# Kernel optimization log

Hardware: AMD Instinct MI355X
Metric: run time of the kernel (lower is better)

Reference implementation:

```python
import jax, jax.numpy as jnp
import numpy as np

R = 16
ALPHA = 16.0
SCALE = ALPHA / max(1, R)  # alpha / max(1, r)


def setup_inputs() -> dict:
    key = jax.random.key(0)
    k1, k2, k3, k4, k5 = jax.random.split(key, 5)
    B, S, D_IN, D_OUT = 4, 4096, 4096, 4096
    x = jax.random.normal(k1, (B, S, D_IN), dtype=jnp.float32)
    weight = jax.random.normal(k2, (D_OUT, D_IN), dtype=jnp.float32) * (1.0 / np.sqrt(D_IN))
    bias = jax.random.normal(k3, (D_OUT,), dtype=jnp.float32)
    lora_A = jax.random.normal(k4, (R, D_IN), dtype=jnp.float32) * (1.0 / np.sqrt(D_IN))
    lora_B = jax.random.normal(k5, (D_OUT, R), dtype=jnp.float32) * (1.0 / np.sqrt(R))
    return {"x": x, "weight": weight, "bias": bias, "lora_A": lora_A, "lora_B": lora_B}


def reference(x, weight, bias, lora_A, lora_B):
    # base = F.linear(x, weight, bias) = x @ W^T + b
    base = jnp.einsum('bsi,oi->bso', x, weight) + bias
    # lora = x @ (B @ A)^T = (x @ A^T) @ B^T  (chained low-rank, same math)
    xa = jnp.einsum('bsi,ri->bsr', x, lora_A)   # [B,S,r]
    lora = jnp.einsum('bsr,or->bso', xa, lora_B)  # [B,S,out]
    return base + SCALE * lora
```

## Files before the change

kernel.cpp:

```cpp
#include <hip/hip_runtime.h>
#include <stdint.h>

#define M_DIM 16384
#define N_DIM 4096
#define K_DIM 4096
#define LORA_SCALE 1.0f

#define BM 256
#define BN 256
#define BK 64
#define NT (K_DIM / BK)

typedef _Float16 half8 __attribute__((ext_vector_type(8)));
typedef float f32x4 __attribute__((ext_vector_type(4)));

__global__ __launch_bounds__(256) void prep_kernel(const float* __restrict__ x,
                                                   _Float16* __restrict__ xb,
                                                   const float* __restrict__ W,
                                                   const float* __restrict__ lA,
                                                   const float* __restrict__ lB,
                                                   _Float16* __restrict__ wp) {
    const int t = threadIdx.x;
    const int WBLK = (N_DIM * K_DIM) / (256 * 8);

    if (blockIdx.x < WBLK) {
        const size_t base = ((size_t)blockIdx.x * 256 + t) * 8;
        const int n = (int)(base >> 12);
        const int k = (int)(base & (K_DIM - 1));
        const int ns = __builtin_amdgcn_readfirstlane(n);
        float Brow[16];
#pragma unroll
        for (int r = 0; r < 16; ++r) Brow[r] = lB[(size_t)ns * 16 + r];

        f32x4 w0 = *(const f32x4*)(W + base);
        f32x4 w1 = *(const f32x4*)(W + base + 4);
        f32x4 d0 = {0.f, 0.f, 0.f, 0.f}, d1 = {0.f, 0.f, 0.f, 0.f};
#pragma unroll
        for (int r = 0; r < 16; ++r) {
            const float* ar = lA + (size_t)r * K_DIM + k;
            f32x4 a0 = *(const f32x4*)ar;
            f32x4 a1 = *(const f32x4*)(ar + 4);
            d0 += Brow[r] * a0;
            d1 += Brow[r] * a1;
        }
        w0 += LORA_SCALE * d0;
        w1 += LORA_SCALE * d1;
        half8 h;
        h[0] = (_Float16)w0[0]; h[1] = (_Float16)w0[1];
        h[2] = (_Float16)w0[2]; h[3] = (_Float16)w0[3];
        h[4] = (_Float16)w1[0]; h[5] = (_Float16)w1[1];
        h[6] = (_Float16)w1[2]; h[7] = (_Float16)w1[3];
        *(half8*)(wp + base) = h;
        return;
    }

    const size_t base = ((size_t)(blockIdx.x - WBLK) * 256 + t) * 8;
    f32x4 a = *(const f32x4*)(x + base);
    f32x4 b = *(const f32x4*)(x + base + 4);
    half8 h;
    h[0] = (_Float16)a[0]; h[1] = (_Float16)a[1];
    h[2] = (_Float16)a[2]; h[3] = (_Float16)a[3];
    h[4] = (_Float16)b[0]; h[5] = (_Float16)b[1];
    h[6] = (_Float16)b[2]; h[7] = (_Float16)b[3];
    *(half8*)(xb + base) = h;
}

__device__ __forceinline__ void load_lds16(const void* g, void* l) {
    __builtin_amdgcn_global_load_lds(
        (const __attribute__((address_space(1))) unsigned int*)(uintptr_t)g,
        (__attribute__((address_space(3))) unsigned int*)(uintptr_t)l,
        16, 0, 0);
}

__global__ __launch_bounds__(512, 2) void gemm256_kernel(const _Float16* __restrict__ A,
                                                         const _Float16* __restrict__ B,
                                                         const float* __restrict__ bias,
                                                         float* __restrict__ C) {
    __shared__ _Float16 As[2][2][256 * 32];
    __shared__ _Float16 Bs[2][2][256 * 32];

    const int tid  = threadIdx.x;
    const int lane = tid & 63;
    const int wave = tid >> 6;
    const int wm   = wave >> 2;
    const int wn   = wave & 3;
    const int quad = lane >> 4;
    const int r16  = lane & 15;
    const int swz  = (quad ^ ((r16 >> 1) & 3)) << 3;

    const int bid = blockIdx.x;
    const int id  = (bid & 7) * 128 + (bid >> 3);
    const int m0  = (id >> 4) * BM;
    const int n0  = (id & 15) * BN;

    const int  srow = tid >> 2;
    const int  scol = (((tid & 3) ^ ((tid >> 3) & 3)) << 3);
    const _Float16* gA = A + (size_t)(m0 + srow) * K_DIM + scol;
    const _Float16* gB = B + (size_t)(n0 + srow) * K_DIM + scol;
    const int ldst0 = tid * 8;
    const int ldst1 = (tid + 512) * 8;

    const int arow = (wm * 128 + r16) * 32 + swz;
    const int brow = (wn * 64 + r16) * 32 + swz;

    f32x4 acc[8][4] = {};
    half8 a[4], b[4];

#define ISSUE_A(DB, KH, T) do { \
        const _Float16* g_ = gA + (size_t)((T) * 64 + (KH) * 32); \
        load_lds16(g_, &As[DB][KH][ldst0]); \
        load_lds16(g_ + (size_t)128 * K_DIM, &As[DB][KH][ldst1]); \
    } while (0)
#define ISSUE_B(DB, KH, T) do { \
        const _Float16* g_ = gB + (size_t)((T) * 64 + (KH) * 32); \
        load_lds16(g_, &Bs[DB][KH][ldst0]); \
        load_lds16(g_ + (size_t)128 * K_DIM, &Bs[DB][KH][ldst1]); \
    } while (0)

#define MID() do { \
        asm volatile("" ::: "memory"); __builtin_amdgcn_sched_barrier(0); \
        __builtin_amdgcn_s_barrier(); \
        asm volatile("s_waitcnt lgkmcnt(0)" ::: "memory"); \
        __builtin_amdgcn_sched_barrier(0); \
        __builtin_amdgcn_s_setprio(1); \
    } while (0)
#define ENDP() do { \
        __builtin_amdgcn_s_setprio(0); \
        asm volatile("" ::: "memory"); __builtin_amdgcn_sched_barrier(0); \
        __builtin_amdgcn_s_barrier(); \
    } while (0)

#define MFMA16(MLO) \
        _Pragma("unroll") \
        for (int i_ = 0; i_ < 4; ++i_) \
            _Pragma("unroll") \
            for (int j_ = 0; j_ < 4; ++j_) \
                acc[(MLO) + i_][j_] = __builtin_amdgcn_mfma_f32_16x16x32_f16( \
                    a[i_], b[j_], acc[(MLO) + i_][j_], 0, 0, 0);

#define PH_BA(DB, KH, ISS) do { \
        _Pragma("unroll") \
        for (int j_ = 0; j_ < 4; ++j_) b[j_] = *(const half8*)&Bs[DB][KH][brow + j_ * 512]; \
        _Pragma("unroll") \
        for (int i_ = 0; i_ < 4; ++i_) a[i_] = *(const half8*)&As[DB][KH][arow + i_ * 512]; \
        ISS; MID(); MFMA16(0) ENDP(); \
    } while (0)
#define PH_A2(DB, KH, ISS) do { \
        _Pragma("unroll") \
        for (int i_ = 0; i_ < 4; ++i_) a[i_] = *(const half8*)&As[DB][KH][arow + (i_ + 4) * 512]; \
        ISS; MID(); MFMA16(4) ENDP(); \
    } while (0)
#define PH_A2L(DB, KH, ISS) do { \
        _Pragma("unroll") \
        for (int i_ = 0; i_ < 4; ++i_) a[i_] = *(const half8*)&As[DB][KH][arow + (i_ + 4) * 512]; \
        ISS; MID(); MFMA16(4) \
    } while (0)

#define TILE(DB, T1, T2) do { \
        PH_BA(DB, 0, ISSUE_A(1 - (DB), 1, T1)); \
        PH_A2(DB, 0, ISSUE_B(DB, 0, T2)); \
        PH_BA(DB, 1, ISSUE_A(DB, 0, T2)); \
        PH_A2L(DB, 1, ISSUE_B(DB, 1, T2)); \
    } while (0)
#define ENDT6() do { \
        __builtin_amdgcn_s_setprio(0); \
        asm volatile("" ::: "memory"); __builtin_amdgcn_sched_barrier(0); \
        asm volatile("s_waitcnt vmcnt(6)" ::: "memory"); \
        __builtin_amdgcn_s_barrier(); \
    } while (0)

    ISSUE_B(0, 0, 0); ISSUE_A(0, 0, 0); ISSUE_B(0, 1, 0); ISSUE_A(0, 1, 0);
    ISSUE_B(1, 0, 1); ISSUE_A(1, 0, 1); ISSUE_B(1, 1, 1);
    asm volatile("s_waitcnt vmcnt(6)" ::: "memory");
    __builtin_amdgcn_s_barrier();

#pragma unroll 1
    for (int ip = 0; ip < 31; ++ip) {
        const int t1 = 2 * ip + 1, t2 = 2 * ip + 2, t3 = 2 * ip + 3;
        TILE(0, t1, t2);
        ENDT6();
        TILE(1, t2, t3);
        ENDT6();
    }
    PH_BA(0, 0, ISSUE_A(1, 1, 63));
    PH_A2(0, 0, (void)0);
    PH_BA(0, 1, (void)0);
    PH_A2L(0, 1, (void)0);
    __builtin_amdgcn_s_setprio(0);
    asm volatile("" ::: "memory"); __builtin_amdgcn_sched_barrier(0);
    asm volatile("s_waitcnt vmcnt(0)" ::: "memory");
    __builtin_amdgcn_s_barrier();
    PH_BA(1, 0, (void)0);
    PH_A2(1, 0, (void)0);
    PH_BA(1, 1, (void)0);
    PH_A2L(1, 1, (void)0);
    __builtin_amdgcn_s_setprio(0);

#undef TILE
#undef ENDT6
#undef PH_BA
#undef PH_A2
#undef PH_A2L
#undef MFMA16
#undef MID
#undef ENDP
#undef ISSUE_A
#undef ISSUE_B

#pragma unroll
    for (int j = 0; j < 4; ++j) {
        const int n = n0 + wn * 64 + j * 16 + r16;
        const float bv = bias[n];
#pragma unroll
        for (int i = 0; i < 8; ++i) {
            const int mbase = m0 + wm * 128 + i * 16 + quad * 4;
#pragma unroll
            for (int r = 0; r < 4; ++r) {
                C[(size_t)(mbase + r) * N_DIM + n] = acc[i][j][r] + bv;
            }
        }
    }
}

extern "C" void kernel_launch(void* const* d_in, const int* in_sizes, int n_in,
                              void* d_out, int out_size, void* d_ws, size_t ws_size,
                              hipStream_t stream) {
    const float* x      = (const float*)d_in[0];
    const float* weight = (const float*)d_in[1];
    const float* bias   = (const float*)d_in[2];
    const float* lora_A = (const float*)d_in[3];
    const float* lora_B = (const float*)d_in[4];
    float* out = (float*)d_out;

    _Float16* xb = (_Float16*)d_ws;
    _Float16* wp = (_Float16*)((char*)d_ws + (size_t)M_DIM * K_DIM * 2);

    const int wblk = (N_DIM * K_DIM) / (256 * 8);
    const int xblk = (int)((M_DIM * (size_t)K_DIM) / (256 * 8));
    prep_kernel<<<dim3(wblk + xblk), dim3(256), 0, stream>>>(x, xb, weight, lora_A, lora_B, wp);
    gemm256_kernel<<<dim3((M_DIM / BM) * (N_DIM / BN)), dim3(512), 0, stream>>>(xb, wp, bias, out);
}
```

Before: 989.5 us.

## Double-buffer LDS fragment registers to overlap reads with MFMA phases

Splits the A/B fragment registers into even/odd sets so the LDS reads for the next phase are issued before the current phase's MFMAs. Partial lgkmcnt waits replace full waits, letting LDS latency hide behind matrix math, and the next tile's first fragments are prefetched at the end of each tile. This raises VGPR usage and makes the wait-count bookkeeping more fragile.

```diff
diff --git a/kernel.cpp b/kernel.cpp
--- a/kernel.cpp
+++ b/kernel.cpp
@@ -72,6 +72,21 @@
         16, 0, 0);
 }
 
+#define BARRIER() do { \
+        asm volatile("" ::: "memory"); \
+        __builtin_amdgcn_sched_barrier(0); \
+        __builtin_amdgcn_s_barrier(); \
+        asm volatile("" ::: "memory"); \
+    } while (0)
+#define WAIT_LGKM(N) do { \
+        asm volatile("s_waitcnt lgkmcnt(" #N ")" ::: "memory"); \
+        __builtin_amdgcn_sched_barrier(0); \
+    } while (0)
+#define WAIT_VM(N) do { \
+        asm volatile("s_waitcnt vmcnt(" #N ")" ::: "memory"); \
+        __builtin_amdgcn_sched_barrier(0); \
+    } while (0)
+
 __global__ __launch_bounds__(512, 2) void gemm256_kernel(const _Float16* __restrict__ A,
                                                          const _Float16* __restrict__ B,
                                                          const float* __restrict__ bias,
@@ -104,7 +119,7 @@
     const int brow = (wn * 64 + r16) * 32 + swz;
 
     f32x4 acc[8][4] = {};
-    half8 a[4], b[4];
+    half8 ae[4], ao[4], be[4], bo[4];
 
 #define ISSUE_A(DB, KH, T) do { \
         const _Float16* g_ = gA + (size_t)((T) * 64 + (KH) * 32); \
@@ -117,93 +132,99 @@
         load_lds16(g_ + (size_t)128 * K_DIM, &Bs[DB][KH][ldst1]); \
     } while (0)
 
-#define MID() do { \
-        asm volatile("" ::: "memory"); __builtin_amdgcn_sched_barrier(0); \
-        __builtin_amdgcn_s_barrier(); \
-        asm volatile("s_waitcnt lgkmcnt(0)" ::: "memory"); \
-        __builtin_amdgcn_sched_barrier(0); \
+#define RD_A4(BUF, DB, KH, MH) \
+        _Pragma("unroll") \
+        for (int i_ = 0; i_ < 4; ++i_) \
+            BUF[i_] = *(const half8*)&As[DB][KH][arow + ((MH) * 4 + i_) * 512];
+#define RD_B4(BUF, DB, KH) \
+        _Pragma("unroll") \
+        for (int j_ = 0; j_ < 4; ++j_) \
+            BUF[j_] = *(const half8*)&Bs[DB][KH][brow + j_ * 512];
+
+#define MFMA16(BB, AA, MLO) \
         __builtin_amdgcn_s_setprio(1); \
-    } while (0)
-#define ENDP() do { \
-        __builtin_amdgcn_s_setprio(0); \
-        asm volatile("" ::: "memory"); __builtin_amdgcn_sched_barrier(0); \
-        __builtin_amdgcn_s_barrier(); \
-    } while (0)
-
-#define MFMA16(MLO) \
         _Pragma("unroll") \
         for (int i_ = 0; i_ < 4; ++i_) \
             _Pragma("unroll") \
             for (int j_ = 0; j_ < 4; ++j_) \
                 acc[(MLO) + i_][j_] = __builtin_amdgcn_mfma_f32_16x16x32_f16( \
-                    a[i_], b[j_], acc[(MLO) + i_][j_], 0, 0, 0);
-
-#define PH_BA(DB, KH, ISS) do { \
-        _Pragma("unroll") \
-        for (int j_ = 0; j_ < 4; ++j_) b[j_] = *(const half8*)&Bs[DB][KH][brow + j_ * 512]; \
-        _Pragma("unroll") \
-        for (int i_ = 0; i_ < 4; ++i_) a[i_] = *(const half8*)&As[DB][KH][arow + i_ * 512]; \
-        ISS; MID(); MFMA16(0) ENDP(); \
-    } while (0)
-#define PH_A2(DB, KH, ISS) do { \
-        _Pragma("unroll") \
-        for (int i_ = 0; i_ < 4; ++i_) a[i_] = *(const half8*)&As[DB][KH][arow + (i_ + 4) * 512]; \
-        ISS; MID(); MFMA16(4) ENDP(); \
-    } while (0)
-#define PH_A2L(DB, KH, ISS) do { \
-        _Pragma("unroll") \
-        for (int i_ = 0; i_ < 4; ++i_) a[i_] = *(const half8*)&As[DB][KH][arow + (i_ + 4) * 512]; \
-        ISS; MID(); MFMA16(4) \
-    } while (0)
-
-#define TILE(DB, T1, T2) do { \
-        PH_BA(DB, 0, ISSUE_A(1 - (DB), 1, T1)); \
-        PH_A2(DB, 0, ISSUE_B(DB, 0, T2)); \
-        PH_BA(DB, 1, ISSUE_A(DB, 0, T2)); \
-        PH_A2L(DB, 1, ISSUE_B(DB, 1, T2)); \
-    } while (0)
-#define ENDT6() do { \
-        __builtin_amdgcn_s_setprio(0); \
-        asm volatile("" ::: "memory"); __builtin_amdgcn_sched_barrier(0); \
-        asm volatile("s_waitcnt vmcnt(6)" ::: "memory"); \
-        __builtin_amdgcn_s_barrier(); \
+                    AA[i_], BB[j_], acc[(MLO) + i_][j_], 0, 0, 0); \
+        __builtin_amdgcn_s_setprio(0);
+
+#define PH0(DB, T1, DOISS) do { \
+        RD_A4(ao, DB, 0, 1); \
+        if (DOISS) ISSUE_A(1 - (DB), 1, T1); \
+        BARRIER(); \
+        WAIT_LGKM(4); \
+        MFMA16(be, ae, 0) \
+        BARRIER(); \
+    } while (0)
+#define PH1(DB, T2, DOISS) do { \
+        RD_B4(bo, DB, 1); \
+        RD_A4(ae, DB, 1, 0); \
+        if (DOISS) ISSUE_B(DB, 0, T2); \
+        BARRIER(); \
+        WAIT_LGKM(8); \
+        MFMA16(be, ao, 4) \
+        BARRIER(); \
+    } while (0)
+#define PH2(DB, T2, DOISS) do { \
+        RD_A4(ao, DB, 1, 1); \
+        if (DOISS) ISSUE_A(DB, 0, T2); \
+        BARRIER(); \
+        WAIT_LGKM(4); \
+        MFMA16(bo, ae, 0) \
+        BARRIER(); \
+    } while (0)
+#define PH3(DB, T2) do { \
+        WAIT_VM(8); \
+        ISSUE_B(DB, 1, T2); \
+        BARRIER(); \
+        RD_B4(be, 1 - (DB), 0); \
+        RD_A4(ae, 1 - (DB), 0, 0); \
+        WAIT_LGKM(8); \
+        MFMA16(bo, ao, 4) \
+        WAIT_VM(6); \
+        BARRIER(); \
     } while (0)
 
     ISSUE_B(0, 0, 0); ISSUE_A(0, 0, 0); ISSUE_B(0, 1, 0); ISSUE_A(0, 1, 0);
     ISSUE_B(1, 0, 1); ISSUE_A(1, 0, 1); ISSUE_B(1, 1, 1);
-    asm volatile("s_waitcnt vmcnt(6)" ::: "memory");
-    __builtin_amdgcn_s_barrier();
+    WAIT_VM(6);
+    BARRIER();
+    RD_B4(be, 0, 0);
+    RD_A4(ae, 0, 0, 0);
 
 #pragma unroll 1
     for (int ip = 0; ip < 31; ++ip) {
-        const int t1 = 2 * ip + 1, t2 = 2 * ip + 2, t3 = 2 * ip + 3;
-        TILE(0, t1, t2);
-        ENDT6();
-        TILE(1, t2, t3);
-        ENDT6();
+        const int t = 2 * ip;
+        PH0(0, t + 1, 1); PH1(0, t + 2, 1); PH2(0, t + 2, 1); PH3(0, t + 2);
+        PH0(1, t + 2, 1); PH1(1, t + 3, 1); PH2(1, t + 3, 1); PH3(1, t + 3);
     }
-    PH_BA(0, 0, ISSUE_A(1, 1, 63));
-    PH_A2(0, 0, (void)0);
-    PH_BA(0, 1, (void)0);
-    PH_A2L(0, 1, (void)0);
-    __builtin_amdgcn_s_setprio(0);
-    asm volatile("" ::: "memory"); __builtin_amdgcn_sched_barrier(0);
-    asm volatile("s_waitcnt vmcnt(0)" ::: "memory");
-    __builtin_amdgcn_s_barrier();
-    PH_BA(1, 0, (void)0);
-    PH_A2(1, 0, (void)0);
-    PH_BA(1, 1, (void)0);
-    PH_A2L(1, 1, (void)0);
-    __builtin_amdgcn_s_setprio(0);
-
-#undef TILE
-#undef ENDT6
-#undef PH_BA
-#undef PH_A2
-#undef PH_A2L
+    PH0(0, 63, 1);
+    PH1(0, 0, 0);
+    PH2(0, 0, 0);
+    WAIT_VM(4);
+    BARRIER();
+    RD_B4(be, 1, 0);
+    RD_A4(ae, 1, 0, 0);
+    WAIT_LGKM(8);
+    MFMA16(bo, ao, 4)
+    WAIT_VM(0);
+    BARRIER();
+    PH0(1, 0, 0);
+    PH1(1, 0, 0);
+    PH2(1, 0, 0);
+    WAIT_LGKM(0);
+    MFMA16(bo, ao, 4)
+
+#undef PH0
+#undef PH1
+#undef PH2
+#undef PH3
 #undef MFMA16
-#undef MID
-#undef ENDP
+#undef RD_A4
+#undef RD_B4
 #undef ISSUE_A
 #undef ISSUE_B
 
```

Result: no change. 995.6 us (+0.6%).

## Shrink GEMM tile to 256x128 with BK=32 and a three-stage LDS ring

Applied to the files above, without the earlier changes.

Replaces the 256x256 tile (eight waves each computing 128x64) with a 256x128 tile (eight waves each computing 64x64) and BK=32 steps. The double-buffered two-half-K pipeline becomes a triple-buffered ring with one barrier per step. Launch bounds ask for 4 blocks per CU to raise occupancy and hide latency. In exchange, arithmetic intensity per block drops, so there is more global and LDS traffic per FLOP and more barriers per unit of work.

```diff
diff --git a/kernel.cpp b/kernel.cpp
--- a/kernel.cpp
+++ b/kernel.cpp
@@ -7,9 +7,9 @@
 #define LORA_SCALE 1.0f
 
 #define BM 256
-#define BN 256
-#define BK 64
-#define NT (K_DIM / BK)
+#define BN 128
+#define BK 32
+#define NSTEP (K_DIM / BK)
 
 typedef _Float16 half8 __attribute__((ext_vector_type(8)));
 typedef float f32x4 __attribute__((ext_vector_type(4)));
@@ -72,26 +72,41 @@
         16, 0, 0);
 }
 
-__global__ __launch_bounds__(512, 2) void gemm256_kernel(const _Float16* __restrict__ A,
+#define BARRIER() do { \
+        asm volatile("" ::: "memory"); \
+        __builtin_amdgcn_sched_barrier(0); \
+        __builtin_amdgcn_s_barrier(); \
+        asm volatile("" ::: "memory"); \
+    } while (0)
+#define WAIT_LGKM0() do { \
+        asm volatile("s_waitcnt lgkmcnt(0)" ::: "memory"); \
+        __builtin_amdgcn_sched_barrier(0); \
+    } while (0)
+#define WAIT_VM(N) do { \
+        asm volatile("s_waitcnt vmcnt(" #N ")" ::: "memory"); \
+        __builtin_amdgcn_sched_barrier(0); \
+    } while (0)
+
+__global__ __launch_bounds__(512, 4) void gemm256_kernel(const _Float16* __restrict__ A,
                                                          const _Float16* __restrict__ B,
                                                          const float* __restrict__ bias,
                                                          float* __restrict__ C) {
-    __shared__ _Float16 As[2][2][256 * 32];
-    __shared__ _Float16 Bs[2][2][256 * 32];
+    __shared__ _Float16 As[3][BM * 32];
+    __shared__ _Float16 Bs[3][BN * 32];
 
     const int tid  = threadIdx.x;
     const int lane = tid & 63;
     const int wave = tid >> 6;
-    const int wm   = wave >> 2;
-    const int wn   = wave & 3;
+    const int wm   = wave >> 1;
+    const int wn   = wave & 1;
     const int quad = lane >> 4;
     const int r16  = lane & 15;
     const int swz  = (quad ^ ((r16 >> 1) & 3)) << 3;
 
     const int bid = blockIdx.x;
-    const int id  = (bid & 7) * 128 + (bid >> 3);
-    const int m0  = (id >> 4) * BM;
-    const int n0  = (id & 15) * BN;
+    const int id  = (bid & 7) * 256 + (bid >> 3);
+    const int m0  = (id >> 5) * BM;
+    const int n0  = (id & 31) * BN;
 
     const int  srow = tid >> 2;
     const int  scol = (((tid & 3) ^ ((tid >> 3) & 3)) << 3);
@@ -100,120 +115,75 @@
     const int ldst0 = tid * 8;
     const int ldst1 = (tid + 512) * 8;
 
-    const int arow = (wm * 128 + r16) * 32 + swz;
+    const int arow = (wm * 64 + r16) * 32 + swz;
     const int brow = (wn * 64 + r16) * 32 + swz;
 
-    f32x4 acc[8][4] = {};
+    f32x4 acc[4][4] = {};
     half8 a[4], b[4];
 
-#define ISSUE_A(DB, KH, T) do { \
-        const _Float16* g_ = gA + (size_t)((T) * 64 + (KH) * 32); \
-        load_lds16(g_, &As[DB][KH][ldst0]); \
-        load_lds16(g_ + (size_t)128 * K_DIM, &As[DB][KH][ldst1]); \
-    } while (0)
-#define ISSUE_B(DB, KH, T) do { \
-        const _Float16* g_ = gB + (size_t)((T) * 64 + (KH) * 32); \
-        load_lds16(g_, &Bs[DB][KH][ldst0]); \
-        load_lds16(g_ + (size_t)128 * K_DIM, &Bs[DB][KH][ldst1]); \
-    } while (0)
-
-#define MID() do { \
-        asm volatile("" ::: "memory"); __builtin_amdgcn_sched_barrier(0); \
-        __builtin_amdgcn_s_barrier(); \
-        asm volatile("s_waitcnt lgkmcnt(0)" ::: "memory"); \
-        __builtin_amdgcn_sched_barrier(0); \
+#define ISSUE(SLOT, T) do { \
+        const _Float16* gA_ = gA + (size_t)(T) * 32; \
+        load_lds16(gA_, &As[SLOT][ldst0]); \
+        load_lds16(gA_ + (size_t)128 * K_DIM, &As[SLOT][ldst1]); \
+        load_lds16(gB + (size_t)(T) * 32, &Bs[SLOT][ldst0]); \
+    } while (0)
+
+#define STEP(SLOT, NXSLOT, TNEXT, DOISS, VMTAIL) do { \
+        _Pragma("unroll") \
+        for (int i_ = 0; i_ < 4; ++i_) a[i_] = *(const half8*)&As[SLOT][arow + i_ * 512]; \
+        _Pragma("unroll") \
+        for (int j_ = 0; j_ < 4; ++j_) b[j_] = *(const half8*)&Bs[SLOT][brow + j_ * 512]; \
+        if (DOISS) ISSUE(NXSLOT, TNEXT); \
+        WAIT_LGKM0(); \
         __builtin_amdgcn_s_setprio(1); \
-    } while (0)
-#define ENDP() do { \
-        __builtin_amdgcn_s_setprio(0); \
-        asm volatile("" ::: "memory"); __builtin_amdgcn_sched_barrier(0); \
-        __builtin_amdgcn_s_barrier(); \
-    } while (0)
-
-#define MFMA16(MLO) \
         _Pragma("unroll") \
         for (int i_ = 0; i_ < 4; ++i_) \
             _Pragma("unroll") \
             for (int j_ = 0; j_ < 4; ++j_) \
-                acc[(MLO) + i_][j_] = __builtin_amdgcn_mfma_f32_16x16x32_f16( \
-                    a[i_], b[j_], acc[(MLO) + i_][j_], 0, 0, 0);
-
-#define PH_BA(DB, KH, ISS) do { \
-        _Pragma("unroll") \
-        for (int j_ = 0; j_ < 4; ++j_) b[j_] = *(const half8*)&Bs[DB][KH][brow + j_ * 512]; \
-        _Pragma("unroll") \
-        for (int i_ = 0; i_ < 4; ++i_) a[i_] = *(const half8*)&As[DB][KH][arow + i_ * 512]; \
-        ISS; MID(); MFMA16(0) ENDP(); \
-    } while (0)
-#define PH_A2(DB, KH, ISS) do { \
-        _Pragma("unroll") \
-        for (int i_ = 0; i_ < 4; ++i_) a[i_] = *(const half8*)&As[DB][KH][arow + (i_ + 4) * 512]; \
-        ISS; MID(); MFMA16(4) ENDP(); \
-    } while (0)
-#define PH_A2L(DB, KH, ISS) do { \
-        _Pragma("unroll") \
-        for (int i_ = 0; i_ < 4; ++i_) a[i_] = *(const half8*)&As[DB][KH][arow + (i_ + 4) * 512]; \
-        ISS; MID(); MFMA16(4) \
-    } while (0)
-
-#define TILE(DB, T1, T2) do { \
-        PH_BA(DB, 0, ISSUE_A(1 - (DB), 1, T1)); \
-        PH_A2(DB, 0, ISSUE_B(DB, 0, T2)); \
-        PH_BA(DB, 1, ISSUE_A(DB, 0, T2)); \
-        PH_A2L(DB, 1, ISSUE_B(DB, 1, T2)); \
-    } while (0)
-#define ENDT6() do { \
+                acc[i_][j_] = __builtin_amdgcn_mfma_f32_16x16x32_f16( \
+                    a[i_], b[j_], acc[i_][j_], 0, 0, 0); \
         __builtin_amdgcn_s_setprio(0); \
-        asm volatile("" ::: "memory"); __builtin_amdgcn_sched_barrier(0); \
-        asm volatile("s_waitcnt vmcnt(6)" ::: "memory"); \
-        __builtin_amdgcn_s_barrier(); \
-    } while (0)
-
-    ISSUE_B(0, 0, 0); ISSUE_A(0, 0, 0); ISSUE_B(0, 1, 0); ISSUE_A(0, 1, 0);
-    ISSUE_B(1, 0, 1); ISSUE_A(1, 0, 1); ISSUE_B(1, 1, 1);
-    asm volatile("s_waitcnt vmcnt(6)" ::: "memory");
-    __builtin_amdgcn_s_barrier();
+        VMTAIL; \
+        BARRIER(); \
+    } while (0)
+
+    ISSUE(0, 0);
+    ISSUE(1, 1);
+    WAIT_VM(3);
+    BARRIER();
 
 #pragma unroll 1
-    for (int ip = 0; ip < 31; ++ip) {
-        const int t1 = 2 * ip + 1, t2 = 2 * ip + 2, t3 = 2 * ip + 3;
-        TILE(0, t1, t2);
-        ENDT6();
-        TILE(1, t2, t3);
-        ENDT6();
-    }
-    PH_BA(0, 0, ISSUE_A(1, 1, 63));
-    PH_A2(0, 0, (void)0);
-    PH_BA(0, 1, (void)0);
-    PH_A2L(0, 1, (void)0);
-    __builtin_amdgcn_s_setprio(0);
-    asm volatile("" ::: "memory"); __builtin_amdgcn_sched_barrier(0);
-    asm volatile("s_waitcnt vmcnt(0)" ::: "memory");
-    __builtin_amdgcn_s_barrier();
-    PH_BA(1, 0, (void)0);
-    PH_A2(1, 0, (void)0);
-    PH_BA(1, 1, (void)0);
-    PH_A2L(1, 1, (void)0);
-    __builtin_amdgcn_s_setprio(0);
-
-#undef TILE
-#undef ENDT6
-#undef PH_BA
-#undef PH_A2
-#undef PH_A2L
-#undef MFMA16
-#undef MID
-#undef ENDP
-#undef ISSUE_A
-#undef ISSUE_B
+    for (int ip = 0; ip < 42; ++ip) {
+        const int t = 3 * ip;
+        STEP(0, 2, t + 2, 1, WAIT_VM(3));
+        STEP(1, 0, t + 3, 1, WAIT_VM(3));
+        STEP(2, 1, t + 4, 1, WAIT_VM(3));
+    }
+    STEP(0, 0, 0, 0, WAIT_VM(0));
+    {
+#pragma unroll
+        for (int i_ = 0; i_ < 4; ++i_) a[i_] = *(const half8*)&As[1][arow + i_ * 512];
+#pragma unroll
+        for (int j_ = 0; j_ < 4; ++j_) b[j_] = *(const half8*)&Bs[1][brow + j_ * 512];
+        WAIT_LGKM0();
+#pragma unroll
+        for (int i_ = 0; i_ < 4; ++i_)
+#pragma unroll
+            for (int j_ = 0; j_ < 4; ++j_)
+                acc[i_][j_] = __builtin_amdgcn_mfma_f32_16x16x32_f16(
+                    a[i_], b[j_], acc[i_][j_], 0, 0, 0);
+    }
+
+#undef STEP
+#undef ISSUE
 
 #pragma unroll
     for (int j = 0; j < 4; ++j) {
         const int n = n0 + wn * 64 + j * 16 + r16;
         const float bv = bias[n];
 #pragma unroll
-        for (int i = 0; i < 8; ++i) {
-            const int mbase = m0 + wm * 128 + i * 16 + quad * 4;
+        for (int i = 0; i < 4; ++i) {
+            const int mbase = m0 + wm * 64 + i * 16 + quad * 4;
 #pragma unroll
             for (int r = 0; r < 4; ++r) {
                 C[(size_t)(mbase + r) * N_DIM + n] = acc[i][j][r] + bv;
```

Result: slower. 1.080 ms (+9.1%).
